# Optimization experiments

Hardware: AMD Instinct MI355X
Metric: run time of the kernel (lower is better)

Reference implementation:

```python
import jax, jax.numpy as jnp
import numpy as np

N_DIM = 1024
HEAD_NUM = 16
HEAD_DIM = N_DIM // HEAD_NUM


def setup_inputs() -> dict:
    key = jax.random.key(0)
    ks = jax.random.split(key, 6)
    s = 1.0 / np.sqrt(N_DIM)
    return {
        "x": jax.random.normal(ks[0], (2, 2048, N_DIM), dtype=jnp.float32),
        "wq": jax.random.uniform(ks[1], (N_DIM, N_DIM), jnp.float32, -s, s),
        "wk": jax.random.uniform(ks[2], (N_DIM, N_DIM), jnp.float32, -s, s),
        "wv": jax.random.uniform(ks[3], (N_DIM, N_DIM), jnp.float32, -s, s),
        "wo": jax.random.uniform(ks[4], (N_DIM, N_DIM), jnp.float32, -s, s),
        "bo": jax.random.uniform(ks[5], (N_DIM,), jnp.float32, -s, s),
    }


def reference(x, wq, wk, wv, wo, bo):
    B, S, D = x.shape
    # torch Linear: y = x @ W.T
    def proj(w):
        return (x @ w.T).reshape(B, S, HEAD_NUM, HEAD_DIM).transpose(0, 2, 1, 3)  # [B,H,S,Dh]
    q, k, v = proj(wq), proj(wk), proj(wv)
    scale = 1.0 / np.sqrt(HEAD_DIM).astype(np.float32)
    scores = jnp.einsum("bhqd,bhkd->bhqk", q, k) * scale  # [B,H,S,S]
    attn = jax.nn.softmax(scores, axis=-1)
    y = jnp.einsum("bhqk,bhkd->bhqd", attn, v)  # [B,H,S,Dh]
    y = y.transpose(0, 2, 1, 3).reshape(B, S, D)
    return y @ wo.T + bo
```

## Files before the change

### kernel.cpp

```cpp
#include <hip/hip_runtime.h>
#include <math.h>

#define B_DIM 2
#define S_DIM 2048
#define D_DIM 1024
#define H_NUM 16
#define DH    64
#define M_DIM (B_DIM * S_DIM)

typedef __attribute__((ext_vector_type(8))) short short8;
typedef __attribute__((ext_vector_type(4))) short short4v;
typedef __attribute__((ext_vector_type(4))) float float4v;
typedef __attribute__((ext_vector_type(4))) unsigned short ushort4v;
typedef unsigned short ushort;

static __device__ __forceinline__ ushort f2bf(float f) {
    unsigned u = __float_as_uint(f);
    u += 0x7fffu + ((u >> 16) & 1u);
    return (ushort)(u >> 16);
}

static __device__ __forceinline__ float fexp2(float x) {
#if __has_builtin(__builtin_amdgcn_exp2f)
    return __builtin_amdgcn_exp2f(x);
#else
    return exp2f(x);
#endif
}

static __device__ __forceinline__ unsigned cvtpk_bf16(float lo, float hi) {
    unsigned r;
    asm("v_cvt_pk_bf16_f32 %0, %1, %2" : "=v"(r) : "v"(lo), "v"(hi));
    return r;
}

static __device__ __forceinline__ void gload_lds16(const void* g, void* l) {
    __builtin_amdgcn_global_load_lds(
        (const __attribute__((address_space(1))) void*)g,
        (__attribute__((address_space(3))) void*)l, 16, 0, 0);
}

__global__ __launch_bounds__(256)
void cast_all(const float* __restrict__ x,  const float* __restrict__ wq,
              const float* __restrict__ wk, const float* __restrict__ wv,
              const float* __restrict__ wo, ushort* __restrict__ dst)
{
    const int i = blockIdx.x * 256 + threadIdx.x;
    const float4* s;
    int off;
    if      (i < 1048576) { s = (const float4*)x;  off = 0;       }
    else if (i < 1310720) { s = (const float4*)wq; off = 1048576; }
    else if (i < 1572864) { s = (const float4*)wk; off = 1310720; }
    else if (i < 1835008) { s = (const float4*)wv; off = 1572864; }
    else                  { s = (const float4*)wo; off = 1835008; }
    const float4 v = s[i - off];
    ushort4v o;
    o[0] = f2bf(v.x); o[1] = f2bf(v.y); o[2] = f2bf(v.z); o[3] = f2bf(v.w);
    ((ushort4v*)dst)[i] = o;
}

__global__ __launch_bounds__(256)
void gemm_bf16(const ushort* __restrict__ A, const ushort* __restrict__ B,
               ushort* __restrict__ Qh, ushort* __restrict__ Kh,
               ushort* __restrict__ Vt)
{
    __shared__ ushort Asm[128 * 64];
    __shared__ ushort Bsm[128 * 64];

    const int K = 1024;
    const int lin = blockIdx.y * 24 + blockIdx.x;
    const int swz = (lin & 7) * 96 + (lin >> 3);
    const int n0 = (swz % 24) * 128;
    const int m0 = (swz / 24) * 128;
    const int t    = threadIdx.x;
    const int w    = t >> 6;
    const int lane = t & 63;
    const int n    = lane & 15;
    const int quad = lane >> 4;
    const int wm = w >> 1, wn = w & 1;

    const int l8 = lane >> 3;
    const int sg = (lane & 7) ^ l8;

    const int fswz[2] = { ((0 * 4 + quad) ^ (n & 7)) * 8,
                          ((1 * 4 + quad) ^ (n & 7)) * 8 };

    float4v acc[4][4];
#pragma unroll
    for (int mt = 0; mt < 4; ++mt)
#pragma unroll
        for (int nt = 0; nt < 4; ++nt) acc[mt][nt] = (float4v){0.f, 0.f, 0.f, 0.f};

    for (int kt = 0; kt < K; kt += 64) {
#pragma unroll
        for (int i = 0; i < 4; ++i) {
            gload_lds16(&A[(size_t)(m0 + w * 32 + i * 8 + l8) * K + kt + sg * 8],
                        &Asm[(w * 32 + i * 8) * 64]);
            gload_lds16(&B[(size_t)(n0 + w * 32 + i * 8 + l8) * K + kt + sg * 8],
                        &Bsm[(w * 32 + i * 8) * 64]);
        }
        __syncthreads();

        short8 af[4][2], bfr[4][2];
#pragma unroll
        for (int mt = 0; mt < 4; ++mt)
#pragma unroll
            for (int kk = 0; kk < 2; ++kk)
                af[mt][kk] = *(const short8*)&Asm[(wm * 64 + mt * 16 + n) * 64 + fswz[kk]];
#pragma unroll
        for (int nt = 0; nt < 4; ++nt)
#pragma unroll
            for (int kk = 0; kk < 2; ++kk)
                bfr[nt][kk] = *(const short8*)&Bsm[(wn * 64 + nt * 16 + n) * 64 + fswz[kk]];

#pragma unroll
        for (int mt = 0; mt < 4; ++mt)
#pragma unroll
            for (int nt = 0; nt < 4; ++nt) {
                acc[mt][nt] = __builtin_amdgcn_mfma_f32_16x16x32_bf16(
                    af[mt][0], bfr[nt][0], acc[mt][nt], 0, 0, 0);
                acc[mt][nt] = __builtin_amdgcn_mfma_f32_16x16x32_bf16(
                    af[mt][1], bfr[nt][1], acc[mt][nt], 0, 0, 0);
            }
        __syncthreads();
    }

    const int wid = n0 >> 10;
    ushort* dstQK = (wid == 0) ? Qh : Kh;
    const float qs = (wid == 0) ? 0.1803368801f : 1.0f;
#pragma unroll
    for (int mt = 0; mt < 4; ++mt) {
        const int m = m0 + wm * 64 + mt * 16 + quad * 4;
        const int b = m >> 11, s = m & (S_DIM - 1);
#pragma unroll
        for (int nt = 0; nt < 4; ++nt) {
            const int ng = (n0 & 1023) + wn * 64 + nt * 16 + n;
            const int h = ng >> 6, d = ng & 63;
            const int bh = b * H_NUM + h;
            if (wid < 2) {
#pragma unroll
                for (int r = 0; r < 4; ++r)
                    dstQK[(((size_t)bh * S_DIM + s + r) << 6) + d] =
                        f2bf(acc[mt][nt][r] * qs);
            } else {
                ushort4v p;
#pragma unroll
                for (int r = 0; r < 4; ++r) p[r] = f2bf(acc[mt][nt][r]);
                *(ushort4v*)&Vt[(((size_t)bh * DH + d) << 11) + s] = p;
            }
        }
    }
}

__global__ __launch_bounds__(256)
void gemm_out(const ushort* __restrict__ A, const ushort* __restrict__ B,
              float* __restrict__ Of, const float* __restrict__ bias)
{
    __shared__ ushort Asm[128 * 64];
    __shared__ ushort Bsm[64 * 64];

    const int K = 1024;
    const int lin = blockIdx.y * 16 + blockIdx.x;
    const int swz = (lin & 7) * 64 + (lin >> 3);
    const int n0 = (swz % 16) * 64;
    const int m0 = (swz / 16) * 128;
    const int t    = threadIdx.x;
    const int w    = t >> 6;
    const int lane = t & 63;
    const int n    = lane & 15;
    const int quad = lane >> 4;
    const int wm = w >> 1, wn = w & 1;

    const int l8 = lane >> 3;
    const int sg = (lane & 7) ^ l8;
    const int fswz[2] = { ((0 * 4 + quad) ^ (n & 7)) * 8,
                          ((1 * 4 + quad) ^ (n & 7)) * 8 };

    float4v acc[4][2];
#pragma unroll
    for (int mt = 0; mt < 4; ++mt)
#pragma unroll
        for (int nt = 0; nt < 2; ++nt) acc[mt][nt] = (float4v){0.f, 0.f, 0.f, 0.f};

    for (int kt = 0; kt < K; kt += 64) {
#pragma unroll
        for (int i = 0; i < 4; ++i)
            gload_lds16(&A[(size_t)(m0 + w * 32 + i * 8 + l8) * K + kt + sg * 8],
                        &Asm[(w * 32 + i * 8) * 64]);
#pragma unroll
        for (int i = 0; i < 2; ++i)
            gload_lds16(&B[(size_t)(n0 + w * 16 + i * 8 + l8) * K + kt + sg * 8],
                        &Bsm[(w * 16 + i * 8) * 64]);
        __syncthreads();

        short8 af[4][2], bfr[2][2];
#pragma unroll
        for (int mt = 0; mt < 4; ++mt)
#pragma unroll
            for (int kk = 0; kk < 2; ++kk)
                af[mt][kk] = *(const short8*)&Asm[(wm * 64 + mt * 16 + n) * 64 + fswz[kk]];
#pragma unroll
        for (int nt = 0; nt < 2; ++nt)
#pragma unroll
            for (int kk = 0; kk < 2; ++kk)
                bfr[nt][kk] = *(const short8*)&Bsm[(wn * 32 + nt * 16 + n) * 64 + fswz[kk]];

#pragma unroll
        for (int mt = 0; mt < 4; ++mt)
#pragma unroll
            for (int nt = 0; nt < 2; ++nt) {
                acc[mt][nt] = __builtin_amdgcn_mfma_f32_16x16x32_bf16(
                    af[mt][0], bfr[nt][0], acc[mt][nt], 0, 0, 0);
                acc[mt][nt] = __builtin_amdgcn_mfma_f32_16x16x32_bf16(
                    af[mt][1], bfr[nt][1], acc[mt][nt], 0, 0, 0);
            }
        __syncthreads();
    }

#pragma unroll
    for (int mt = 0; mt < 4; ++mt) {
        const int m = m0 + wm * 64 + mt * 16 + quad * 4;
#pragma unroll
        for (int nt = 0; nt < 2; ++nt) {
            const int ng = n0 + wn * 32 + nt * 16 + n;
            const float bv = bias[ng];
#pragma unroll
            for (int r = 0; r < 4; ++r)
                Of[(size_t)(m + r) * D_DIM + ng] = acc[mt][nt][r] + bv;
        }
    }
}

__global__ __launch_bounds__(256)
void attn_mfma(const ushort* __restrict__ Qh, const ushort* __restrict__ Kh,
               const ushort* __restrict__ Vt, ushort* __restrict__ Yh)
{
    __shared__ ushort Ksm[2][64 * 64];
    __shared__ ushort Vsm[2][64 * 64];

    const int w    = threadIdx.x >> 6;
    const int lane = threadIdx.x & 63;
    const int n    = lane & 15;
    const int quad = lane >> 4;

    const int wave_id = blockIdx.x * 4 + w;
    const int bh    = wave_id >> 6;
    const int qbase = (wave_id & 63) * 32;
    const int b     = bh >> 4;
    const int h     = bh & (H_NUM - 1);

    const ushort* Qb = Qh + (((size_t)bh * S_DIM) << 6);
    const ushort* Kb = Kh + (((size_t)bh * S_DIM) << 6);
    const ushort* Vb = Vt + (((size_t)bh * DH) << 11);

    const int l8 = lane >> 3;
    const int sg = (lane & 7) ^ l8;

    short8 qa[2][2];
#pragma unroll
    for (int mt = 0; mt < 2; ++mt)
#pragma unroll
        for (int kc = 0; kc < 2; ++kc)
            qa[mt][kc] = *(const short8*)&Qb[((size_t)(qbase + mt * 16 + n) << 6) + kc * 32 + quad * 8];

    float4v O[2][4];
    float   mrow[2], lrow[2];
#pragma unroll
    for (int mt = 0; mt < 2; ++mt) {
#pragma unroll
        for (int nt = 0; nt < 4; ++nt) O[mt][nt] = (float4v){0.f, 0.f, 0.f, 0.f};
        mrow[mt] = -1e30f; lrow[mt] = 0.f;
    }

    const int fswz[2] = { ((0 * 4 + quad) ^ (n & 7)) * 8,
                          ((1 * 4 + quad) ^ (n & 7)) * 8 };
    const int h4 = (quad & 1) * 4;
    const int q2 = quad >> 1;
    int vswz[2][2];
#pragma unroll
    for (int kc = 0; kc < 2; ++kc)
#pragma unroll
        for (int cc = 0; cc < 2; ++cc)
            vswz[kc][cc] = (((4 * kc + 2 * cc + q2) ^ (n & 7)) << 3) + h4;

#pragma unroll
    for (int i = 0; i < 2; ++i) {
        gload_lds16(&Kb[(size_t)(w * 16 + i * 8 + l8) * 64 + sg * 8],
                    &Ksm[0][(w * 16 + i * 8) * 64]);
        gload_lds16(&Vb[(size_t)(w * 16 + i * 8 + l8) * 2048 + sg * 8],
                    &Vsm[0][(w * 16 + i * 8) * 64]);
    }

    for (int kb = 0; kb < S_DIM / 64; ++kb) {
        __syncthreads();
        const int cur = kb & 1;
        if (kb + 1 < S_DIM / 64) {
            const int key1 = (kb + 1) * 64;
            const int nxt  = cur ^ 1;
#pragma unroll
            for (int i = 0; i < 2; ++i) {
                gload_lds16(&Kb[(size_t)(key1 + w * 16 + i * 8 + l8) * 64 + sg * 8],
                            &Ksm[nxt][(w * 16 + i * 8) * 64]);
                gload_lds16(&Vb[(size_t)(w * 16 + i * 8 + l8) * 2048 + key1 + sg * 8],
                            &Vsm[nxt][(w * 16 + i * 8) * 64]);
            }
        }

        short8 kf[4][2];
#pragma unroll
        for (int ct = 0; ct < 4; ++ct)
#pragma unroll
            for (int kc = 0; kc < 2; ++kc)
                kf[ct][kc] = *(const short8*)&Ksm[cur][(ct * 16 + n) * 64 + fswz[kc]];

        float4v s[2][4];
        __builtin_amdgcn_s_setprio(1);
#pragma unroll
        for (int mt = 0; mt < 2; ++mt)
#pragma unroll
            for (int ct = 0; ct < 4; ++ct) {
                float4v a = (float4v){0.f, 0.f, 0.f, 0.f};
                a = __builtin_amdgcn_mfma_f32_16x16x32_bf16(kf[ct][0], qa[mt][0], a, 0, 0, 0);
                a = __builtin_amdgcn_mfma_f32_16x16x32_bf16(kf[ct][1], qa[mt][1], a, 0, 0, 0);
                s[mt][ct] = a;
            }
        __builtin_amdgcn_s_setprio(0);

        short8 vf[4][2];
#pragma unroll
        for (int nt = 0; nt < 4; ++nt) {
            const int rb = (nt * 16 + n) * 64;
#pragma unroll
            for (int kc = 0; kc < 2; ++kc) {
                const short4v g0 = *(const short4v*)&Vsm[cur][rb + vswz[kc][0]];
                const short4v g1 = *(const short4v*)&Vsm[cur][rb + vswz[kc][1]];
                vf[nt][kc] = __builtin_shufflevector(g0, g1, 0, 1, 2, 3, 4, 5, 6, 7);
            }
        }

#pragma unroll
        for (int mt = 0; mt < 2; ++mt) {
            float lm = s[mt][0][0];
#pragma unroll
            for (int ct = 0; ct < 4; ++ct)
#pragma unroll
                for (int r = 0; r < 4; ++r)
                    lm = fmaxf(lm, s[mt][ct][r]);
            lm = fmaxf(lm, __shfl_xor(lm, 16, 64));
            lm = fmaxf(lm, __shfl_xor(lm, 32, 64));

            const bool ev = lm > mrow[mt] + 8.0f;
            if (__any(ev)) {
                const float mnew  = ev ? lm : mrow[mt];
                const float alpha = fexp2(mrow[mt] - mnew);
                mrow[mt] = mnew;
                lrow[mt] *= alpha;
                const int ai = __float_as_int(alpha);
                float av[4];
#pragma unroll
                for (int r = 0; r < 4; ++r)
                    av[r] = __int_as_float(
                        __builtin_amdgcn_ds_bpermute(4 * (quad * 4 + r), ai));
#pragma unroll
                for (int nt = 0; nt < 4; ++nt)
#pragma unroll
                    for (int r = 0; r < 4; ++r) O[mt][nt][r] *= av[r];
            }

            float pv[4][4];
            float lsum = 0.f;
#pragma unroll
            for (int ct = 0; ct < 4; ++ct)
#pragma unroll
                for (int r = 0; r < 4; ++r) {
                    const float p = fexp2(s[mt][ct][r] - mrow[mt]);
                    pv[ct][r] = p;
                    lsum += p;
                }
            lrow[mt] += lsum;

            union { unsigned u[4]; short8 s8; } pk[2];
#pragma unroll
            for (int kc = 0; kc < 2; ++kc) {
                pk[kc].u[0] = cvtpk_bf16(pv[2 * kc][0],     pv[2 * kc][1]);
                pk[kc].u[1] = cvtpk_bf16(pv[2 * kc][2],     pv[2 * kc][3]);
                pk[kc].u[2] = cvtpk_bf16(pv[2 * kc + 1][0], pv[2 * kc + 1][1]);
                pk[kc].u[3] = cvtpk_bf16(pv[2 * kc + 1][2], pv[2 * kc + 1][3]);
            }

            __builtin_amdgcn_s_setprio(1);
#pragma unroll
            for (int nt = 0; nt < 4; ++nt) {
                O[mt][nt] = __builtin_amdgcn_mfma_f32_16x16x32_bf16(pk[0].s8, vf[nt][0], O[mt][nt], 0, 0, 0);
                O[mt][nt] = __builtin_amdgcn_mfma_f32_16x16x32_bf16(pk[1].s8, vf[nt][1], O[mt][nt], 0, 0, 0);
            }
            __builtin_amdgcn_s_setprio(0);
        }
    }

#pragma unroll
    for (int mt = 0; mt < 2; ++mt) {
        float ls = lrow[mt];
        ls += __shfl_xor(ls, 16, 64);
        ls += __shfl_xor(ls, 32, 64);
        const float linv = 1.f / ls;
        const int  li = __float_as_int(linv);
        float lv[4];
#pragma unroll
        for (int r = 0; r < 4; ++r)
            lv[r] = __int_as_float(
                __builtin_amdgcn_ds_bpermute(4 * (quad * 4 + r), li));
#pragma unroll
        for (int nt = 0; nt < 4; ++nt)
#pragma unroll
            for (int r = 0; r < 4; ++r) {
                const int q = qbase + mt * 16 + quad * 4 + r;
                Yh[((size_t)(b * S_DIM + q) << 10) + h * DH + nt * 16 + n] =
                    f2bf(O[mt][nt][r] * lv[r]);
            }
    }
}

extern "C" void kernel_launch(void* const* d_in, const int* in_sizes, int n_in,
                              void* d_out, int out_size, void* d_ws, size_t ws_size,
                              hipStream_t stream)
{
    const float* x  = (const float*)d_in[0];
    const float* wq = (const float*)d_in[1];
    const float* wk = (const float*)d_in[2];
    const float* wv = (const float*)d_in[3];
    const float* wo = (const float*)d_in[4];
    const float* bo = (const float*)d_in[5];
    float* out = (float*)d_out;

    const size_t MD = (size_t)M_DIM * D_DIM;
    const size_t WD = (size_t)D_DIM * D_DIM;
    ushort* xh  = (ushort*)d_ws;
    ushort* Wh  = xh + MD;
    ushort* Woh = Wh + 3 * WD;
    ushort* Qh  = Woh + WD;
    ushort* Kh  = Qh + MD;
    ushort* Vt  = Kh + MD;
    ushort* Yh  = Vt + MD;
    if (ws_size < 48u * 1024u * 1024u) return;

    dim3 blk(256);
    cast_all<<<dim3(8192), blk, 0, stream>>>(x, wq, wk, wv, wo, xh);

    gemm_bf16<<<dim3(24, 32), blk, 0, stream>>>(xh, Wh, Qh, Kh, Vt);
    attn_mfma<<<dim3(512), blk, 0, stream>>>(Qh, Kh, Vt, Yh);
    gemm_out<<<dim3(16, 32), blk, 0, stream>>>(Yh, Woh, out, bo);
}
```

Measured before the change: 207.8 us.

## Double-buffer LDS tiles in projection GEMMs and raise MFMA wave priority

Both the QKV projection GEMM and the output GEMM now use two LDS buffers. The next K-tile's global-to-LDS loads are issued right after a single barrier per iteration, so they overlap with the MFMA work on the current tile, and the trailing barrier is removed. The MFMA section is wrapped in s_setprio raises to favour issuing matrix instructions. In exchange, LDS use per block doubles (64 KB for the QKV kernel), which can lower occupancy.

```diff
diff --git a/kernel.cpp b/kernel.cpp
--- a/kernel.cpp
+++ b/kernel.cpp
@@ -64,10 +64,11 @@
                ushort* __restrict__ Qh, ushort* __restrict__ Kh,
                ushort* __restrict__ Vt)
 {
-    __shared__ ushort Asm[128 * 64];
-    __shared__ ushort Bsm[128 * 64];
+    __shared__ ushort Asm[2][128 * 64];
+    __shared__ ushort Bsm[2][128 * 64];
 
     const int K = 1024;
+    const int NT = 16;
     const int lin = blockIdx.y * 24 + blockIdx.x;
     const int swz = (lin & 7) * 96 + (lin >> 3);
     const int n0 = (swz % 24) * 128;
@@ -91,28 +92,42 @@
 #pragma unroll
         for (int nt = 0; nt < 4; ++nt) acc[mt][nt] = (float4v){0.f, 0.f, 0.f, 0.f};
 
-    for (int kt = 0; kt < K; kt += 64) {
-#pragma unroll
-        for (int i = 0; i < 4; ++i) {
-            gload_lds16(&A[(size_t)(m0 + w * 32 + i * 8 + l8) * K + kt + sg * 8],
-                        &Asm[(w * 32 + i * 8) * 64]);
-            gload_lds16(&B[(size_t)(n0 + w * 32 + i * 8 + l8) * K + kt + sg * 8],
-                        &Bsm[(w * 32 + i * 8) * 64]);
-        }
+#pragma unroll
+    for (int i = 0; i < 4; ++i) {
+        gload_lds16(&A[(size_t)(m0 + w * 32 + i * 8 + l8) * K + sg * 8],
+                    &Asm[0][(w * 32 + i * 8) * 64]);
+        gload_lds16(&B[(size_t)(n0 + w * 32 + i * 8 + l8) * K + sg * 8],
+                    &Bsm[0][(w * 32 + i * 8) * 64]);
+    }
+
+    for (int kt6 = 0; kt6 < NT; ++kt6) {
         __syncthreads();
+        const int cur = kt6 & 1;
+        if (kt6 + 1 < NT) {
+            const int kt1 = (kt6 + 1) * 64;
+            const int nxt = cur ^ 1;
+#pragma unroll
+            for (int i = 0; i < 4; ++i) {
+                gload_lds16(&A[(size_t)(m0 + w * 32 + i * 8 + l8) * K + kt1 + sg * 8],
+                            &Asm[nxt][(w * 32 + i * 8) * 64]);
+                gload_lds16(&B[(size_t)(n0 + w * 32 + i * 8 + l8) * K + kt1 + sg * 8],
+                            &Bsm[nxt][(w * 32 + i * 8) * 64]);
+            }
+        }
 
         short8 af[4][2], bfr[4][2];
 #pragma unroll
         for (int mt = 0; mt < 4; ++mt)
 #pragma unroll
             for (int kk = 0; kk < 2; ++kk)
-                af[mt][kk] = *(const short8*)&Asm[(wm * 64 + mt * 16 + n) * 64 + fswz[kk]];
+                af[mt][kk] = *(const short8*)&Asm[cur][(wm * 64 + mt * 16 + n) * 64 + fswz[kk]];
 #pragma unroll
         for (int nt = 0; nt < 4; ++nt)
 #pragma unroll
             for (int kk = 0; kk < 2; ++kk)
-                bfr[nt][kk] = *(const short8*)&Bsm[(wn * 64 + nt * 16 + n) * 64 + fswz[kk]];
-
+                bfr[nt][kk] = *(const short8*)&Bsm[cur][(wn * 64 + nt * 16 + n) * 64 + fswz[kk]];
+
+        __builtin_amdgcn_s_setprio(1);
 #pragma unroll
         for (int mt = 0; mt < 4; ++mt)
 #pragma unroll
@@ -122,7 +137,7 @@
                 acc[mt][nt] = __builtin_amdgcn_mfma_f32_16x16x32_bf16(
                     af[mt][1], bfr[nt][1], acc[mt][nt], 0, 0, 0);
             }
-        __syncthreads();
+        __builtin_amdgcn_s_setprio(0);
     }
 
     const int wid = n0 >> 10;
@@ -156,10 +171,11 @@
 void gemm_out(const ushort* __restrict__ A, const ushort* __restrict__ B,
               float* __restrict__ Of, const float* __restrict__ bias)
 {
-    __shared__ ushort Asm[128 * 64];
-    __shared__ ushort Bsm[64 * 64];
+    __shared__ ushort Asm[2][128 * 64];
+    __shared__ ushort Bsm[2][64 * 64];
 
     const int K = 1024;
+    const int NT = 16;
     const int lin = blockIdx.y * 16 + blockIdx.x;
     const int swz = (lin & 7) * 64 + (lin >> 3);
     const int n0 = (swz % 16) * 64;
@@ -182,29 +198,44 @@
 #pragma unroll
         for (int nt = 0; nt < 2; ++nt) acc[mt][nt] = (float4v){0.f, 0.f, 0.f, 0.f};
 
-    for (int kt = 0; kt < K; kt += 64) {
-#pragma unroll
-        for (int i = 0; i < 4; ++i)
-            gload_lds16(&A[(size_t)(m0 + w * 32 + i * 8 + l8) * K + kt + sg * 8],
-                        &Asm[(w * 32 + i * 8) * 64]);
-#pragma unroll
-        for (int i = 0; i < 2; ++i)
-            gload_lds16(&B[(size_t)(n0 + w * 16 + i * 8 + l8) * K + kt + sg * 8],
-                        &Bsm[(w * 16 + i * 8) * 64]);
+#pragma unroll
+    for (int i = 0; i < 4; ++i)
+        gload_lds16(&A[(size_t)(m0 + w * 32 + i * 8 + l8) * K + sg * 8],
+                    &Asm[0][(w * 32 + i * 8) * 64]);
+#pragma unroll
+    for (int i = 0; i < 2; ++i)
+        gload_lds16(&B[(size_t)(n0 + w * 16 + i * 8 + l8) * K + sg * 8],
+                    &Bsm[0][(w * 16 + i * 8) * 64]);
+
+    for (int kt6 = 0; kt6 < NT; ++kt6) {
         __syncthreads();
+        const int cur = kt6 & 1;
+        if (kt6 + 1 < NT) {
+            const int kt1 = (kt6 + 1) * 64;
+            const int nxt = cur ^ 1;
+#pragma unroll
+            for (int i = 0; i < 4; ++i)
+                gload_lds16(&A[(size_t)(m0 + w * 32 + i * 8 + l8) * K + kt1 + sg * 8],
+                            &Asm[nxt][(w * 32 + i * 8) * 64]);
+#pragma unroll
+            for (int i = 0; i < 2; ++i)
+                gload_lds16(&B[(size_t)(n0 + w * 16 + i * 8 + l8) * K + kt1 + sg * 8],
+                            &Bsm[nxt][(w * 16 + i * 8) * 64]);
+        }
 
         short8 af[4][2], bfr[2][2];
 #pragma unroll
         for (int mt = 0; mt < 4; ++mt)
 #pragma unroll
             for (int kk = 0; kk < 2; ++kk)
-                af[mt][kk] = *(const short8*)&Asm[(wm * 64 + mt * 16 + n) * 64 + fswz[kk]];
+                af[mt][kk] = *(const short8*)&Asm[cur][(wm * 64 + mt * 16 + n) * 64 + fswz[kk]];
 #pragma unroll
         for (int nt = 0; nt < 2; ++nt)
 #pragma unroll
             for (int kk = 0; kk < 2; ++kk)
-                bfr[nt][kk] = *(const short8*)&Bsm[(wn * 32 + nt * 16 + n) * 64 + fswz[kk]];
-
+                bfr[nt][kk] = *(const short8*)&Bsm[cur][(wn * 32 + nt * 16 + n) * 64 + fswz[kk]];
+
+        __builtin_amdgcn_s_setprio(1);
 #pragma unroll
         for (int mt = 0; mt < 4; ++mt)
 #pragma unroll
@@ -214,7 +245,7 @@
                 acc[mt][nt] = __builtin_amdgcn_mfma_f32_16x16x32_bf16(
                     af[mt][1], bfr[nt][1], acc[mt][nt], 0, 0, 0);
             }
-        __syncthreads();
+        __builtin_amdgcn_s_setprio(0);
     }
 
 #pragma unroll
```

Result: faster. 202.8 us (-2.4%).
